# Performance work log

Hardware: AMD Instinct MI355X
Metric: run time of the kernel (lower is better)

Reference implementation:

```python
import jax, jax.numpy as jnp
import numpy as np

N_M, N_C, D, H, E, EL = 200000, 50000, 128, 64, 1000000, 100000


def gat_conv(h_src, h_dst, W_src, W_dst, a_src, a_dst, b, src, dst, n_dst):
    # PyG GATConv (heads=1): project, per-edge attention logit, segment softmax over dst, weighted scatter-sum.
    hs = h_src @ W_src                      # [Ns, H]
    hd = h_dst @ W_dst                      # [Nd, H]
    al_s = hs @ a_src                       # [Ns]
    al_d = hd @ a_dst                       # [Nd]
    alpha = jax.nn.leaky_relu(al_s[src] + al_d[dst], 0.2)   # [E]
    m = jax.ops.segment_max(alpha, dst, num_segments=n_dst)
    m = jnp.where(jnp.isfinite(m), m, 0.0)
    e = jnp.exp(alpha - m[dst])
    denom = jax.ops.segment_sum(e, dst, num_segments=n_dst)
    w = e / jnp.maximum(denom[dst], 1e-16)
    out = jax.ops.segment_sum(w[:, None] * hs[src], dst, num_segments=n_dst)
    return out + b


def setup_inputs() -> dict:
    key = jax.random.key(0)
    ks = jax.random.split(key, 32)
    p = lambda k, s: (jax.random.normal(k, s, jnp.float32) * 0.1)
    inp = {
        'x_m': jax.random.normal(ks[0], (N_M, D), jnp.float32),
        'x_c': jax.random.normal(ks[1], (N_C, D), jnp.float32),
        'src_mc': jax.random.randint(ks[2], (E,), 0, N_M, jnp.int32),
        'dst_mc': jax.random.randint(ks[3], (E,), 0, N_C, jnp.int32),
        'src_cm': jax.random.randint(ks[4], (E,), 0, N_C, jnp.int32),
        'dst_cm': jax.random.randint(ks[5], (E,), 0, N_M, jnp.int32),
        'row': jax.random.randint(ks[6], (EL,), 0, N_M, jnp.int32),
        'col': jax.random.randint(ks[7], (EL,), 0, N_C, jnp.int32),
        'W1s_mc': p(ks[8], (D, H)), 'W1d_mc': p(ks[9], (D, H)),
        'a1s_mc': p(ks[10], (H,)), 'a1d_mc': p(ks[11], (H,)), 'b1_mc': p(ks[12], (H,)),
        'W1s_cm': p(ks[13], (D, H)), 'W1d_cm': p(ks[14], (D, H)),
        'a1s_cm': p(ks[15], (H,)), 'a1d_cm': p(ks[16], (H,)), 'b1_cm': p(ks[17], (H,)),
        'W2s_mc': p(ks[18], (H, H)), 'W2d_mc': p(ks[19], (H, H)),
        'a2s_mc': p(ks[20], (H,)), 'a2d_mc': p(ks[21], (H,)), 'b2_mc': p(ks[22], (H,)),
        'W2s_cm': p(ks[23], (H, H)), 'W2d_cm': p(ks[24], (H, H)),
        'a2s_cm': p(ks[25], (H,)), 'a2d_cm': p(ks[26], (H,)), 'b2_cm': p(ks[27], (H,)),
        'Wd1': p(ks[28], (2 * H, H)), 'bd1': p(ks[29], (H,)),
        'Wd2': p(ks[30], (H, 2)), 'bd2': p(ks[31], (2,)),
    }
    return inp


def reference(x_m, x_c, src_mc, dst_mc, src_cm, dst_cm, row, col,
              W1s_mc, W1d_mc, a1s_mc, a1d_mc, b1_mc,
              W1s_cm, W1d_cm, a1s_cm, a1d_cm, b1_cm,
              W2s_mc, W2d_mc, a2s_mc, a2d_mc, b2_mc,
              W2s_cm, W2d_cm, a2s_cm, a2d_cm, b2_cm,
              Wd1, bd1, Wd2, bd2):
    # Layer 1: materials receive only via concepts->materials edges; concepts via materials->concepts.
    z_c = jax.nn.relu(gat_conv(x_m, x_c, W1s_mc, W1d_mc, a1s_mc, a1d_mc, b1_mc, src_mc, dst_mc, N_C))
    z_m = jax.nn.relu(gat_conv(x_c, x_m, W1s_cm, W1d_cm, a1s_cm, a1d_cm, b1_cm, src_cm, dst_cm, N_M))
    # Layer 2 (no activation)
    z_c2 = gat_conv(z_m, z_c, W2s_mc, W2d_mc, a2s_mc, a2d_mc, b2_mc, src_mc, dst_mc, N_C)
    z_m2 = gat_conv(z_c, z_m, W2s_cm, W2d_cm, a2s_cm, a2d_cm, b2_cm, src_cm, dst_cm, N_M)
    # Edge decoder: gather-concat + 2-layer MLP (no activation between, per source)
    z = jnp.concatenate([z_m2[row], z_c2[col]], axis=-1)   # [EL, 2H]
    z = z @ Wd1 + bd1
    z = z @ Wd2 + bd2
    return z.reshape(-1)
```

## Files before the change

### kernel.cpp

```cpp
#include <hip/hip_runtime.h>
#include <hip/hip_fp16.h>
#include <cstdint>
#include <cstddef>

typedef _Float16 f16x8 __attribute__((ext_vector_type(8)));
typedef float f32x4 __attribute__((ext_vector_type(4)));

__device__ __forceinline__ float exp_am8(float a) {
    return __builtin_amdgcn_exp2f(fmaf(a, 1.442695040888963f, -11.541560327111707f));
}

__global__ void prep_all(
    const float* __restrict__ Wa0, const float* __restrict__ Wb0, _Float16* __restrict__ P0,
    const float* __restrict__ Wa1, const float* __restrict__ Wb1, _Float16* __restrict__ P1,
    const float* __restrict__ Wd1, const float* __restrict__ bd1,
    const float* __restrict__ Wd2, const float* __restrict__ bd2,
    const float* __restrict__ b2_cm, const float* __restrict__ b2_mc,
    const float* __restrict__ W2s_mc, const float* __restrict__ a2s_mc,
    const float* __restrict__ W2d_cm, const float* __restrict__ a2d_cm,
    const float* __restrict__ W2s_cm, const float* __restrict__ a2s_cm,
    const float* __restrict__ W2d_mc, const float* __restrict__ a2d_mc,
    float* __restrict__ Wc, float* __restrict__ bc, float* __restrict__ bq,
    float4* __restrict__ foldA, float4* __restrict__ foldB,
    int* __restrict__ bcnt_base) {
    __shared__ float WcS[256];
    int b = blockIdx.x;
    int t = threadIdx.x;
    if (b < 128) {
        const float* Wa; const float* Wb; _Float16* Wp; int lb;
        if (b < 64) { Wa = Wa0; Wb = Wb0; Wp = P0; lb = b; }
        else        { Wa = Wa1; Wb = Wb1; Wp = P1; lb = b - 64; }
        constexpr int K = 128;
        constexpr int NKB = K / 32;
        int i = lb * 256 + t;
        if (i >= 128 * K) return;
        int k = i >> 7, c = i & 127;
        float v = (c < 64) ? Wa[k * 64 + c] : Wb[k * 64 + (c - 64)];
        int ct = c >> 4, lr = c & 15, kb = k >> 5, lk = (k & 31) >> 3, e = k & 7;
        Wp[((ct * NKB + kb) * 64 + (lr + 16 * lk)) * 8 + e] = (_Float16)v;
    } else if (b == 128) {
        int k = t >> 1, c = t & 1;
        float s = 0.f;
        for (int j = 0; j < 64; ++j) s += Wd1[k * 64 + j] * Wd2[j * 2 + c];
        Wc[k * 2 + c] = s;
        WcS[k * 2 + c] = s;
        if (k == 0) {
            float bv = bd2[c];
            for (int j = 0; j < 64; ++j) bv += bd1[j] * Wd2[j * 2 + c];
            bc[c] = bv;
        }
        __syncthreads();
        if (t < 2) {
            float v = 0.f;
            for (int j = 0; j < 64; ++j) v += b2_cm[j] * WcS[j * 2 + t];
            bq[t] = v;
        } else if (t < 4) {
            int cc = t - 2;
            float v = 0.f;
            for (int j = 0; j < 64; ++j) v += b2_mc[j] * WcS[(64 + j) * 2 + cc];
            bq[t] = v;
        }
        if (t < 64) {
            int j = t;
            float fa = 0.f, fd = 0.f, qx = 0.f, qy = 0.f;
            for (int cc = 0; cc < 64; ++cc) {
                float ws = W2s_mc[j * 64 + cc];
                fa += ws * a2s_mc[cc];
                qx += ws * WcS[(64 + cc) * 2 + 0];
                qy += ws * WcS[(64 + cc) * 2 + 1];
                fd += W2d_cm[j * 64 + cc] * a2d_cm[cc];
            }
            foldA[j] = make_float4(fa, fd, qx, qy);
        } else if (t < 128) {
            int j = t - 64;
            float fa = 0.f, fd = 0.f, qx = 0.f, qy = 0.f;
            for (int cc = 0; cc < 64; ++cc) {
                float ws = W2s_cm[j * 64 + cc];
                fa += ws * a2s_cm[cc];
                qx += ws * WcS[cc * 2 + 0];
                qy += ws * WcS[cc * 2 + 1];
                fd += W2d_mc[j * 64 + cc] * a2d_mc[cc];
            }
            foldB[j] = make_float4(fa, fd, qx, qy);
        }
    } else {
        bcnt_base[t] = 0;
        bcnt_base[t + 256] = 0;
    }
}

#define XPAD 72

__device__ __forceinline__ void proj_body(const float* __restrict__ X, int N,
                                          const _Float16* __restrict__ Wp,
                                          const float* __restrict__ a0v,
                                          const float* __restrict__ a1v,
                                          __half* __restrict__ out0,
                                          float* __restrict__ al0,
                                          float* __restrict__ al1,
                                          char* smem, int blk) {
    constexpr int K = 128;
    _Float16* Wlds = (_Float16*)smem;
    _Float16* Xs = (_Float16*)(smem + 32768);
    int t = threadIdx.x;
    constexpr int NV = (128 * K) / 8;
#pragma unroll
    for (int i = t; i < NV; i += 512)
        ((uint4*)Wlds)[i] = ((const uint4*)Wp)[i];

    int rt = blk * 128;
    int wv = t >> 6, lane = t & 63, lr = lane & 15, lk = lane >> 4;
    int row = rt + wv * 16 + lr;
    int xrow = t >> 4;
    int xcp = t & 15;

    f32x4 acc[8];
#pragma unroll
    for (int i = 0; i < 8; ++i) acc[i] = f32x4{0.f, 0.f, 0.f, 0.f};

    const f16x8* Wf = (const f16x8*)Wlds;
#pragma unroll
    for (int half = 0; half < 2; ++half) {
        __syncthreads();
#pragma unroll
        for (int pass = 0; pass < 4; ++pass) {
            int r = pass * 32 + xrow;
            int grow = rt + r;
            if (grow >= N) grow = N - 1;
            float4 v = *(const float4*)(X + (size_t)grow * K + half * 64 + xcp * 4);
            __half2 h01 = __floats2half2_rn(v.x, v.y);
            __half2 h23 = __floats2half2_rn(v.z, v.w);
            uint2 pk;
            pk.x = *(const unsigned int*)&h01;
            pk.y = *(const unsigned int*)&h23;
            *(uint2*)&Xs[r * XPAD + xcp * 4] = pk;
        }
        __syncthreads();
#pragma unroll
        for (int kb = 0; kb < 2; ++kb) {
            f16x8 bf = *(const f16x8*)&Xs[(wv * 16 + lr) * XPAD + kb * 32 + lk * 8];
            int kbb = half * 2 + kb;
#pragma unroll
            for (int ct = 0; ct < 8; ++ct) {
                acc[ct] = __builtin_amdgcn_mfma_f32_16x16x32_f16(
                    Wf[(ct * 4 + kbb) * 64 + lane], bf, acc[ct], 0, 0, 0);
            }
        }
    }

    float p0 = 0.f, p1 = 0.f;
#pragma unroll
    for (int ct = 0; ct < 4; ++ct) {
        float4 aq = ((const float4*)a0v)[ct * 4 + lk];
        f32x4 v = acc[ct];
        p0 += v[0] * aq.x + v[1] * aq.y + v[2] * aq.z + v[3] * aq.w;
    }
#pragma unroll
    for (int ct = 0; ct < 4; ++ct) {
        float4 aq = ((const float4*)a1v)[ct * 4 + lk];
        f32x4 v = acc[4 + ct];
        p1 += v[0] * aq.x + v[1] * aq.y + v[2] * aq.z + v[3] * aq.w;
    }
    p0 += __shfl_xor(p0, 16); p0 += __shfl_xor(p0, 32);
    p1 += __shfl_xor(p1, 16); p1 += __shfl_xor(p1, 32);
    if (row < N) {
#pragma unroll
        for (int ct = 0; ct < 4; ++ct) {
            f32x4 v = acc[ct];
            __half2 h01 = __floats2half2_rn(v[0], v[1]);
            __half2 h23 = __floats2half2_rn(v[2], v[3]);
            uint2 pk;
            pk.x = *(const unsigned int*)&h01;
            pk.y = *(const unsigned int*)&h23;
            *(uint2*)(out0 + ((size_t)row << 6) + ct * 16 + lk * 4) = pk;
        }
        if (lane < 16) { al0[row] = p0; al1[row] = p1; }
    }
}

__global__ __launch_bounds__(512) void fused_proj_hist(
    const float* __restrict__ Xm, int Nm, const _Float16* __restrict__ WpA,
    const float* __restrict__ a0A, const float* __restrict__ a1A,
    __half* __restrict__ outA, float* __restrict__ al0A, float* __restrict__ al1A, int nbm,
    const float* __restrict__ Xc, int Nc, const _Float16* __restrict__ WpB,
    const float* __restrict__ a0B, const float* __restrict__ a1B,
    __half* __restrict__ outB, float* __restrict__ al0B, float* __restrict__ al1B, int nbc,
    const int* __restrict__ dmc, int* __restrict__ bcnt_mc, int shA,
    const int* __restrict__ dcm, int* __restrict__ bcnt_cm, int shB, int E, int nblk) {
    extern __shared__ __align__(16) char smem[];
    int b = blockIdx.x;
    if (b < nbm) {
        proj_body(Xm, Nm, WpA, a0A, a1A, outA, al0A, al1A, smem, b);
        return;
    }
    b -= nbm;
    if (b < nbc) {
        proj_body(Xc, Nc, WpB, a0B, a1B, outB, al0B, al1B, smem, b);
        return;
    }
    b -= nbc;
    int* h = (int*)smem;
    const int* dst; int* bcnt; int sh; int base;
    if (b < nblk) { dst = dmc; bcnt = bcnt_mc; sh = shA; base = b * 4096; }
    else { dst = dcm; bcnt = bcnt_cm; sh = shB; base = (b - nblk) * 4096; }
    int t = threadIdx.x;
    if (t < 256) h[t] = 0;
    __syncthreads();
#pragma unroll
    for (int j = 0; j < 8; ++j) {
        int i = base + j * 512 + t;
        if (i < E) atomicAdd(&h[dst[i] >> sh], 1);
    }
    __syncthreads();
    if (t < 256) {
        int c = h[t];
        if (c > 0) atomicAdd(&bcnt[t], c);
    }
}

__global__ void bucket_scan(const int* __restrict__ bcntA, int nbkA,
                            int* __restrict__ bbaseA, int* __restrict__ bcurA,
                            int* __restrict__ offA, int nA,
                            const int* __restrict__ bcntB, int nbkB,
                            int* __restrict__ bbaseB, int* __restrict__ bcurB,
                            int* __restrict__ offB, int nB, int E) {
    int t = threadIdx.x;
    if (t == 0) {
        int run = 0;
        for (int i = 0; i < nbkA; ++i) { bbaseA[i] = run; bcurA[i] = run; run += bcntA[i]; }
        bbaseA[nbkA] = run;
        offA[nA] = E;
    }
    if (t == 64) {
        int run = 0;
        for (int i = 0; i < nbkB; ++i) { bbaseB[i] = run; bcurB[i] = run; run += bcntB[i]; }
        bbaseB[nbkB] = run;
        offB[nB] = E;
    }
}

__global__ __launch_bounds__(256) void bucket_scatter(
    const int* __restrict__ srcA, const int* __restrict__ dstA,
    int* __restrict__ bcurA, unsigned* __restrict__ pairsA,
    const int* __restrict__ srcB, const int* __restrict__ dstB,
    int* __restrict__ bcurB, unsigned* __restrict__ pairsB,
    int E, int nblkA, int shA, int shB, int srcbits) {
    __shared__ int bcnt[256];
    __shared__ int bbase[256];
    const int* src; const int* dst; int* bcur; unsigned* pairs; int sh; int base;
    if ((int)blockIdx.x < nblkA) {
        src = srcA; dst = dstA; bcur = bcurA; pairs = pairsA; sh = shA;
        base = blockIdx.x * 4096;
    } else {
        src = srcB; dst = dstB; bcur = bcurB; pairs = pairsB; sh = shB;
        base = (blockIdx.x - nblkA) * 4096;
    }
    int t = threadIdx.x;
    int msk = (1 << sh) - 1;
    bcnt[t] = 0;
    __syncthreads();
    int sreg[16], dreg[16];
#pragma unroll
    for (int j = 0; j < 16; ++j) {
        int i = base + j * 256 + t;
        if (i < E) {
            sreg[j] = src[i];
            dreg[j] = dst[i];
            atomicAdd(&bcnt[dreg[j] >> sh], 1);
        } else {
            dreg[j] = -1;
        }
    }
    __syncthreads();
    {
        int c = bcnt[t];
        int g = (c > 0) ? atomicAdd(&bcur[t], c) : 0;
        bbase[t] = g;
        bcnt[t] = 0;
    }
    __syncthreads();
#pragma unroll
    for (int j = 0; j < 16; ++j) {
        if (dreg[j] >= 0) {
            int b = dreg[j] >> sh;
            int r = atomicAdd(&bcnt[b], 1);
            pairs[bbase[b] + r] = ((unsigned)(dreg[j] & msk) << srcbits) | (unsigned)sreg[j];
        }
    }
}

__global__ __launch_bounds__(256) void bucket_expand2(
    const unsigned* __restrict__ pairsA, const int* __restrict__ bbaseA, int nA,
    int* __restrict__ offA, int* __restrict__ csrA, int shA, int nbA,
    const unsigned* __restrict__ pairsB, const int* __restrict__ bbaseB, int nB,
    int* __restrict__ offB, int* __restrict__ csrB, int shB, int srcbits) {
    __shared__ int lcnt[1024];
    __shared__ int red[256];
    const unsigned* pairs; const int* bbase; int n; int* off; int* csr; int sh; int b;
    if ((int)blockIdx.x < nbA) {
        pairs = pairsA; bbase = bbaseA; n = nA; off = offA; csr = csrA; sh = shA;
        b = blockIdx.x;
    } else {
        pairs = pairsB; bbase = bbaseB; n = nB; off = offB; csr = csrB; sh = shB;
        b = blockIdx.x - nbA;
    }
    int dpb = 1 << sh;
    int d0 = b << sh;
    int t = threadIdx.x;
    unsigned smask = (1u << srcbits) - 1u;
    for (int dl = t; dl < dpb; dl += 256) lcnt[dl] = 0;
    __syncthreads();
    int pbeg = bbase[b], pend = bbase[b + 1];
    for (int i = pbeg + t; i < pend; i += 256)
        atomicAdd(&lcnt[pairs[i] >> srcbits], 1);
    __syncthreads();
    int per = (dpb + 255) >> 8;
    int i0 = t * per;
    int s = 0;
    for (int j = 0; j < per; ++j) {
        int dl = i0 + j;
        if (dl < dpb) s += lcnt[dl];
    }
    red[t] = s;
    __syncthreads();
    for (int st = 1; st < 256; st <<= 1) {
        int tmp = (t >= st) ? red[t - st] : 0;
        __syncthreads();
        red[t] += tmp;
        __syncthreads();
    }
    int run = pbeg + red[t] - s;
    for (int j = 0; j < per; ++j) {
        int dl = i0 + j;
        if (dl < dpb) {
            int c = lcnt[dl];
            if (d0 + dl < n) off[d0 + dl] = run;
            lcnt[dl] = run;
            run += c;
        }
    }
    __syncthreads();
    for (int i = pbeg + t; i < pend; i += 256) {
        unsigned p = pairs[i];
        int dl = (int)(p >> srcbits);
        int pos = atomicAdd(&lcnt[dl], 1);
        csr[pos] = (int)(p & smask);
    }
}

#define AGG_CAP 64
#define AGG_PAD 66

__global__ __launch_bounds__(256) void gat_aggregate9f(
    const int* __restrict__ off0, const int* __restrict__ csr0,
    const __half* __restrict__ hs0, const float* __restrict__ als0,
    const float* __restrict__ ald0, const float* __restrict__ bias0,
    const float4* __restrict__ fold0, float* __restrict__ als2_0,
    float* __restrict__ ald2_0, float2* __restrict__ q2_0, int n0,
    const int* __restrict__ off1, const int* __restrict__ csr1,
    const __half* __restrict__ hs1, const float* __restrict__ als1,
    const float* __restrict__ ald1, const float* __restrict__ bias1,
    const float4* __restrict__ fold1, float* __restrict__ als2_1,
    float* __restrict__ ald2_1, float2* __restrict__ q2_1, int n1,
    int nb0) {
    __shared__ uint2 wP[16][AGG_PAD];
    int t = threadIdx.x;
    int slot = t >> 4;
    int sub = t & 15;

    const int* off; const int* csr; const __half* hs; const float* als;
    const float* ald; const float* bias; const float4* fold;
    float* als2; float* ald2; float2* q2; int nd; int b;
    if (blockIdx.x < (unsigned)nb0) {
        b = blockIdx.x;
        off = off0; csr = csr0; hs = hs0; als = als0; ald = ald0; bias = bias0;
        fold = fold0; als2 = als2_0; ald2 = ald2_0; q2 = q2_0; nd = n0;
    } else {
        b = blockIdx.x - nb0;
        off = off1; csr = csr1; hs = hs1; als = als1; ald = ald1; bias = bias1;
        fold = fold1; als2 = als2_1; ald2 = ald2_1; q2 = q2_1; nd = n1;
    }
    int d = b * 16 + slot;
    bool active = d < nd;
    int beg = 0, deg = 0;
    float aldv = 0.f;
    if (active) {
        beg = off[d];
        deg = off[d + 1] - beg;
        aldv = ald[d];
    }
    float4 bl4 = ((const float4*)bias)[sub];
    uint2* WP = wP[slot];

    float sum = 0.f;
    for (int i = sub; i < deg; i += 16) {
        int s = csr[beg + i];
        float a = als[s] + aldv;
        a = (a >= 0.f) ? a : 0.2f * a;
        float w = exp_am8(a);
        sum += w;
        if (i < AGG_CAP) {
            __half hw = __float2half_rn(w);
            __half2 h2 = __half2half2(hw);
            WP[i] = make_uint2(*(const unsigned int*)&h2, (unsigned int)s);
        }
    }
    sum += __shfl_xor(sum, 1);
    sum += __shfl_xor(sum, 2);
    sum += __shfl_xor(sum, 4);
    sum += __shfl_xor(sum, 8);
    float inv = 1.f / fmaxf(sum, 1e-16f);

    int dc = deg < AGG_CAP ? deg : AGG_CAP;
    const uint2* hs4 = (const uint2*)hs;
    __half2 z = __floats2half2_rn(0.f, 0.f);
    __half2 aA = z, aB = z, aC = z, aD = z;
    int i = 0;
    for (; i + 8 <= dc; i += 8) {
        uint4 q0 = *(const uint4*)&WP[i];
        uint4 q1 = *(const uint4*)&WP[i + 2];
        uint4 q2r = *(const uint4*)&WP[i + 4];
        uint4 q3 = *(const uint4*)&WP[i + 6];
        uint2 v0 = hs4[(size_t)q0.y * 16 + sub];
        uint2 v1 = hs4[(size_t)q0.w * 16 + sub];
        uint2 v2 = hs4[(size_t)q1.y * 16 + sub];
        uint2 v3 = hs4[(size_t)q1.w * 16 + sub];
        uint2 v4 = hs4[(size_t)q2r.y * 16 + sub];
        uint2 v5 = hs4[(size_t)q2r.w * 16 + sub];
        uint2 v6 = hs4[(size_t)q3.y * 16 + sub];
        uint2 v7 = hs4[(size_t)q3.w * 16 + sub];
        aA = __hfma2(*(const __half2*)&q0.x, *(const __half2*)&v0.x, aA);
        aB = __hfma2(*(const __half2*)&q0.x, *(const __half2*)&v0.y, aB);
        aC = __hfma2(*(const __half2*)&q0.z, *(const __half2*)&v1.x, aC);
        aD = __hfma2(*(const __half2*)&q0.z, *(const __half2*)&v1.y, aD);
        aA = __hfma2(*(const __half2*)&q1.x, *(const __half2*)&v2.x, aA);
        aB = __hfma2(*(const __half2*)&q1.x, *(const __half2*)&v2.y, aB);
        aC = __hfma2(*(const __half2*)&q1.z, *(const __half2*)&v3.x, aC);
        aD = __hfma2(*(const __half2*)&q1.z, *(const __half2*)&v3.y, aD);
        aA = __hfma2(*(const __half2*)&q2r.x, *(const __half2*)&v4.x, aA);
        aB = __hfma2(*(const __half2*)&q2r.x, *(const __half2*)&v4.y, aB);
        aC = __hfma2(*(const __half2*)&q2r.z, *(const __half2*)&v5.x, aC);
        aD = __hfma2(*(const __half2*)&q2r.z, *(const __half2*)&v5.y, aD);
        aA = __hfma2(*(const __half2*)&q3.x, *(const __half2*)&v6.x, aA);
        aB = __hfma2(*(const __half2*)&q3.x, *(const __half2*)&v6.y, aB);
        aC = __hfma2(*(const __half2*)&q3.z, *(const __half2*)&v7.x, aC);
        aD = __hfma2(*(const __half2*)&q3.z, *(const __half2*)&v7.y, aD);
    }
    for (; i + 2 <= dc; i += 2) {
        uint4 q = *(const uint4*)&WP[i];
        uint2 v0 = hs4[(size_t)q.y * 16 + sub];
        uint2 v1 = hs4[(size_t)q.w * 16 + sub];
        aA = __hfma2(*(const __half2*)&q.x, *(const __half2*)&v0.x, aA);
        aB = __hfma2(*(const __half2*)&q.x, *(const __half2*)&v0.y, aB);
        aC = __hfma2(*(const __half2*)&q.z, *(const __half2*)&v1.x, aC);
        aD = __hfma2(*(const __half2*)&q.z, *(const __half2*)&v1.y, aD);
    }
    if (i < dc) {
        uint2 u = WP[i];
        uint2 v = hs4[(size_t)u.y * 16 + sub];
        aA = __hfma2(*(const __half2*)&u.x, *(const __half2*)&v.x, aA);
        aB = __hfma2(*(const __half2*)&u.x, *(const __half2*)&v.y, aB);
    }
    for (int j = AGG_CAP; j < deg; ++j) {
        int s = csr[beg + j];
        float a = als[s] + aldv;
        a = (a >= 0.f) ? a : 0.2f * a;
        __half hw = __float2half_rn(exp_am8(a));
        __half2 w2 = __half2half2(hw);
        uint2 v = hs4[(size_t)s * 16 + sub];
        aA = __hfma2(w2, *(const __half2*)&v.x, aA);
        aB = __hfma2(w2, *(const __half2*)&v.y, aB);
    }
    float2 fA = __half22float2(aA);
    float2 fB = __half22float2(aB);
    float2 fC = __half22float2(aC);
    float2 fD = __half22float2(aD);
    float o0 = (fA.x + fC.x) * inv + bl4.x;
    float o1 = (fA.y + fC.y) * inv + bl4.y;
    float o2 = (fB.x + fD.x) * inv + bl4.z;
    float o3 = (fB.y + fD.y) * inv + bl4.w;
    if (deg == 0) { o0 = bl4.x; o1 = bl4.y; o2 = bl4.z; o3 = bl4.w; }
    o0 = fmaxf(o0, 0.f); o1 = fmaxf(o1, 0.f);
    o2 = fmaxf(o2, 0.f); o3 = fmaxf(o3, 0.f);

    float4 f0 = fold[4 * sub + 0];
    float4 f1 = fold[4 * sub + 1];
    float4 f2 = fold[4 * sub + 2];
    float4 f3 = fold[4 * sub + 3];
    float a0 = o0 * f0.x + o1 * f1.x + o2 * f2.x + o3 * f3.x;
    float a1 = o0 * f0.y + o1 * f1.y + o2 * f2.y + o3 * f3.y;
    float a2 = o0 * f0.z + o1 * f1.z + o2 * f2.z + o3 * f3.z;
    float a3 = o0 * f0.w + o1 * f1.w + o2 * f2.w + o3 * f3.w;
#pragma unroll
    for (int o = 1; o < 16; o <<= 1) {
        a0 += __shfl_xor(a0, o);
        a1 += __shfl_xor(a1, o);
        a2 += __shfl_xor(a2, o);
        a3 += __shfl_xor(a3, o);
    }
    if (active && sub == 0) {
        als2[d] = a0;
        ald2[d] = a1;
        q2[d] = make_float2(a2, a3);
    }
}

__global__ __launch_bounds__(256) void gat_aggregate10p(
    const int* __restrict__ off0, const int* __restrict__ csr0,
    const float2* __restrict__ q0, const float* __restrict__ als0,
    const float* __restrict__ ald0, const float2* __restrict__ bqp,
    float2* __restrict__ out0, int n0,
    const int* __restrict__ off1, const int* __restrict__ csr1,
    const float2* __restrict__ q1, const float* __restrict__ als1,
    const float* __restrict__ ald1,
    float2* __restrict__ out1, int n1,
    int nb0) {
    const int* off; const int* csr; const float2* qt; const float* als;
    const float* ald; float2 bq; float2* outp; int nd; int b;
    if (blockIdx.x < (unsigned)nb0) {
        b = blockIdx.x;
        off = off0; csr = csr0; qt = q0; als = als0; ald = ald0; bq = bqp[1];
        outp = out0; nd = n0;
    } else {
        b = blockIdx.x - nb0;
        off = off1; csr = csr1; qt = q1; als = als1; ald = ald1; bq = bqp[0];
        outp = out1; nd = n1;
    }
    int d = b * 256 + threadIdx.x;
    if (d >= nd) return;
    int beg = off[d], end = off[d + 1];
    float aldv = ald[d];
    float sum = 0.f, ax = 0.f, ay = 0.f;
    int i = beg;
    for (; i + 2 <= end; i += 2) {
        int s0 = csr[i], s1 = csr[i + 1];
        float a0 = als[s0] + aldv;
        float a1 = als[s1] + aldv;
        float2 v0 = qt[s0];
        float2 v1 = qt[s1];
        a0 = (a0 >= 0.f) ? a0 : 0.2f * a0;
        a1 = (a1 >= 0.f) ? a1 : 0.2f * a1;
        float w0 = exp_am8(a0);
        float w1 = exp_am8(a1);
        sum += w0 + w1;
        ax = fmaf(w0, v0.x, ax); ay = fmaf(w0, v0.y, ay);
        ax = fmaf(w1, v1.x, ax); ay = fmaf(w1, v1.y, ay);
    }
    if (i < end) {
        int s = csr[i];
        float a = als[s] + aldv;
        a = (a >= 0.f) ? a : 0.2f * a;
        float w = exp_am8(a);
        float2 v = qt[s];
        sum += w;
        ax = fmaf(w, v.x, ax); ay = fmaf(w, v.y, ay);
    }
    float inv = 1.f / fmaxf(sum, 1e-16f);
    outp[d] = make_float2(ax * inv + bq.x, ay * inv + bq.y);
}

__global__ __launch_bounds__(256) void decoder4_kernel(const int* __restrict__ row,
                                                       const int* __restrict__ col,
                                                       const float2* __restrict__ pm,
                                                       const float2* __restrict__ pc,
                                                       const float* __restrict__ bc,
                                                       float* __restrict__ out, int EL) {
    int e = blockIdx.x * 256 + threadIdx.x;
    if (e >= EL) return;
    float2 a = pm[row[e]];
    float2 b = pc[col[e]];
    *(float2*)(out + 2 * (size_t)e) = make_float2(a.x + b.x + bc[0], a.y + b.y + bc[1]);
}

extern "C" void kernel_launch(void* const* d_in, const int* in_sizes, int n_in,
                              void* d_out, int out_size, void* d_ws, size_t ws_size,
                              hipStream_t stream) {
    const int D = 128;
    const float* x_m    = (const float*)d_in[0];
    const float* x_c    = (const float*)d_in[1];
    const int*   src_mc = (const int*)d_in[2];
    const int*   dst_mc = (const int*)d_in[3];
    const int*   src_cm = (const int*)d_in[4];
    const int*   dst_cm = (const int*)d_in[5];
    const int*   rowi   = (const int*)d_in[6];
    const int*   coli   = (const int*)d_in[7];
    const float* W1s_mc = (const float*)d_in[8];
    const float* W1d_mc = (const float*)d_in[9];
    const float* a1s_mc = (const float*)d_in[10];
    const float* a1d_mc = (const float*)d_in[11];
    const float* b1_mc  = (const float*)d_in[12];
    const float* W1s_cm = (const float*)d_in[13];
    const float* W1d_cm = (const float*)d_in[14];
    const float* a1s_cm = (const float*)d_in[15];
    const float* a1d_cm = (const float*)d_in[16];
    const float* b1_cm  = (const float*)d_in[17];
    const float* W2s_mc = (const float*)d_in[18];
    const float* W2d_mc = (const float*)d_in[19];
    const float* a2s_mc = (const float*)d_in[20];
    const float* a2d_mc = (const float*)d_in[21];
    const float* b2_mc  = (const float*)d_in[22];
    const float* W2s_cm = (const float*)d_in[23];
    const float* W2d_cm = (const float*)d_in[24];
    const float* a2s_cm = (const float*)d_in[25];
    const float* a2d_cm = (const float*)d_in[26];
    const float* b2_cm  = (const float*)d_in[27];
    const float* Wd1    = (const float*)d_in[28];
    const float* bd1    = (const float*)d_in[29];
    const float* Wd2    = (const float*)d_in[30];
    const float* bd2    = (const float*)d_in[31];

    const int N_M = in_sizes[0] / D;
    const int N_C = in_sizes[1] / D;
    const int E   = in_sizes[2];
    const int EL  = in_sizes[6];
    float* out = (float*)d_out;

    uint8_t* base = (uint8_t*)d_ws;
    size_t off = 0;
    auto carve = [&](size_t bytes) -> void* {
        void* p = base + off;
        off += (bytes + 255) & ~(size_t)255;
        return p;
    };
    __half* hsA_h = (__half*)carve((size_t)N_M * 64 * 2);
    __half* hsB_h = (__half*)carve((size_t)N_C * 64 * 2);
    float2* qA    = (float2*)carve((size_t)N_M * 8);
    float2* qB    = (float2*)carve((size_t)N_C * 8);
    float2* pm_m  = (float2*)carve((size_t)N_M * 8);
    float2* pm_c  = (float2*)carve((size_t)N_C * 8);
    float* als_mc = (float*)carve((size_t)N_M * 4);
    float* ald_cm = (float*)carve((size_t)N_M * 4);
    float* als_cm = (float*)carve((size_t)N_C * 4);
    float* ald_mc = (float*)carve((size_t)N_C * 4);
    float* als2_mc = (float*)carve((size_t)N_M * 4);
    float* ald2_cm = (float*)carve((size_t)N_M * 4);
    float* als2_cm = (float*)carve((size_t)N_C * 4);
    float* ald2_mc = (float*)carve((size_t)N_C * 4);
    int* off_mc = (int*)carve((size_t)(N_C + 1) * 4);
    int* off_cm = (int*)carve((size_t)(N_M + 1) * 4);
    int* csr_mc = (int*)carve((size_t)E * 4);
    int* csr_cm = (int*)carve((size_t)E * 4);
    unsigned* pairs_mc = (unsigned*)carve((size_t)E * 4);
    unsigned* pairs_cm = (unsigned*)carve((size_t)E * 4);
    int* bcnt_base = (int*)carve(512 * 4);
    int* bcnt_mc = bcnt_base;
    int* bcnt_cm = bcnt_base + 256;
    int* bbase_mc = (int*)carve(257 * 4);
    int* bbase_cm = (int*)carve(257 * 4);
    int* bcur_mc = (int*)carve(256 * 4);
    int* bcur_cm = (int*)carve(256 * 4);
    _Float16* wp1A = (_Float16*)carve(128 * 128 * 2);
    _Float16* wp1B = (_Float16*)carve(128 * 128 * 2);
    float* Wc = (float*)carve(256 * 4);
    float* bc = (float*)carve(256);
    float* bq = (float*)carve(256);
    float2* bq2 = (float2*)bq;
    float4* foldA = (float4*)carve(64 * 16);
    float4* foldB = (float4*)carve(64 * 16);

    int shA = 0; while (((N_C + (1 << shA) - 1) >> shA) > 256) shA++;
    int shB = 0; while (((N_M + (1 << shB) - 1) >> shB) > 256) shB++;
    int nbkA = (N_C + (1 << shA) - 1) >> shA;
    int nbkB = (N_M + (1 << shB) - 1) >> shB;
    int maxN = N_M > N_C ? N_M : N_C;
    int srcbits = 1; while ((1 << srcbits) < maxN) srcbits++;

    prep_all<<<130, 256, 0, stream>>>(W1s_mc, W1d_cm, wp1A, W1s_cm, W1d_mc, wp1B,
                                      Wd1, bd1, Wd2, bd2, b2_cm, b2_mc,
                                      W2s_mc, a2s_mc, W2d_cm, a2d_cm,
                                      W2s_cm, a2s_cm, W2d_mc, a2d_mc,
                                      Wc, bc, bq, foldA, foldB, bcnt_base);

    int nbm = (N_M + 127) / 128;
    int nbc = (N_C + 127) / 128;
    int nblk = (E + 4095) / 4096;
    size_t smem_bytes = 32768 + (size_t)128 * XPAD * 2;
    fused_proj_hist<<<nbm + nbc + 2 * nblk, 512, smem_bytes, stream>>>(
        x_m, N_M, wp1A, a1s_mc, a1d_cm, hsA_h, als_mc, ald_cm, nbm,
        x_c, N_C, wp1B, a1s_cm, a1d_mc, hsB_h, als_cm, ald_mc, nbc,
        dst_mc, bcnt_mc, shA, dst_cm, bcnt_cm, shB, E, nblk);

    bucket_scan<<<1, 128, 0, stream>>>(bcnt_mc, nbkA, bbase_mc, bcur_mc, off_mc, N_C,
                                       bcnt_cm, nbkB, bbase_cm, bcur_cm, off_cm, N_M, E);
    bucket_scatter<<<2 * nblk, 256, 0, stream>>>(
        src_mc, dst_mc, bcur_mc, pairs_mc,
        src_cm, dst_cm, bcur_cm, pairs_cm, E, nblk, shA, shB, srcbits);
    bucket_expand2<<<nbkA + nbkB, 256, 0, stream>>>(
        pairs_mc, bbase_mc, N_C, off_mc, csr_mc, shA, nbkA,
        pairs_cm, bbase_cm, N_M, off_cm, csr_cm, shB, srcbits);

    int nb_c16 = (N_C + 15) / 16;
    int nb_m16 = (N_M + 15) / 16;

    gat_aggregate9f<<<nb_c16 + nb_m16, 256, 0, stream>>>(
        off_mc, csr_mc, hsA_h, als_mc, ald_mc, b1_mc, foldB, als2_cm, ald2_mc, qB, N_C,
        off_cm, csr_cm, hsB_h, als_cm, ald_cm, b1_cm, foldA, als2_mc, ald2_cm, qA, N_M,
        nb_c16);

    int nb_c256 = (N_C + 255) / 256;
    int nb_m256 = (N_M + 255) / 256;
    gat_aggregate10p<<<nb_c256 + nb_m256, 256, 0, stream>>>(
        off_mc, csr_mc, qA, als2_mc, ald2_mc, bq2, pm_c, N_C,
        off_cm, csr_cm, qB, als2_cm, ald2_cm, pm_m, N_M, nb_c256);

    decoder4_kernel<<<(EL + 255) / 256, 256, 0, stream>>>(rowi, coli, pm_m, pm_c, bc, out, EL);
}
```

Before: 198.8 us.

## Keep projection weights in registers and split output columns across waves

Measured after the change: 197.4 us. Within noise of the previous version (-0.7%).

```diff
diff --git a/kernel.cpp b/kernel.cpp
--- a/kernel.cpp
+++ b/kernel.cpp
@@ -100,25 +100,26 @@
                                           float* __restrict__ al1,
                                           char* smem, int blk) {
     constexpr int K = 128;
-    _Float16* Wlds = (_Float16*)smem;
-    _Float16* Xs = (_Float16*)(smem + 32768);
+    _Float16* Xs = (_Float16*)smem;
+    float* red0 = (float*)(smem + 128 * XPAD * 2);
+    float* red1 = red0 + 128;
     int t = threadIdx.x;
-    constexpr int NV = (128 * K) / 8;
-#pragma unroll
-    for (int i = t; i < NV; i += 512)
-        ((uint4*)Wlds)[i] = ((const uint4*)Wp)[i];
-
+    int wv = t >> 6, lane = t & 63, lr = lane & 15, lk = lane >> 4;
     int rt = blk * 128;
-    int wv = t >> 6, lane = t & 63, lr = lane & 15, lk = lane >> 4;
-    int row = rt + wv * 16 + lr;
     int xrow = t >> 4;
     int xcp = t & 15;
 
+    f16x8 wfr[4];
+#pragma unroll
+    for (int kbb = 0; kbb < 4; ++kbb)
+        wfr[kbb] = ((const f16x8*)Wp)[(wv * 4 + kbb) * 64 + lane];
+
+    if (t < 128) { red0[t] = 0.f; red1[t] = 0.f; }
+
     f32x4 acc[8];
 #pragma unroll
     for (int i = 0; i < 8; ++i) acc[i] = f32x4{0.f, 0.f, 0.f, 0.f};
 
-    const f16x8* Wf = (const f16x8*)Wlds;
 #pragma unroll
     for (int half = 0; half < 2; ++half) {
         __syncthreads();
@@ -137,44 +138,40 @@
         }
         __syncthreads();
 #pragma unroll
-        for (int kb = 0; kb < 2; ++kb) {
-            f16x8 bf = *(const f16x8*)&Xs[(wv * 16 + lr) * XPAD + kb * 32 + lk * 8];
-            int kbb = half * 2 + kb;
-#pragma unroll
-            for (int ct = 0; ct < 8; ++ct) {
-                acc[ct] = __builtin_amdgcn_mfma_f32_16x16x32_f16(
-                    Wf[(ct * 4 + kbb) * 64 + lane], bf, acc[ct], 0, 0, 0);
+        for (int rt8 = 0; rt8 < 8; ++rt8) {
+#pragma unroll
+            for (int kb = 0; kb < 2; ++kb) {
+                f16x8 bf = *(const f16x8*)&Xs[(rt8 * 16 + lr) * XPAD + kb * 32 + lk * 8];
+                acc[rt8] = __builtin_amdgcn_mfma_f32_16x16x32_f16(
+                    wfr[half * 2 + kb], bf, acc[rt8], 0, 0, 0);
             }
         }
     }
 
-    float p0 = 0.f, p1 = 0.f;
-#pragma unroll
-    for (int ct = 0; ct < 4; ++ct) {
-        float4 aq = ((const float4*)a0v)[ct * 4 + lk];
-        f32x4 v = acc[ct];
-        p0 += v[0] * aq.x + v[1] * aq.y + v[2] * aq.z + v[3] * aq.w;
-    }
-#pragma unroll
-    for (int ct = 0; ct < 4; ++ct) {
-        float4 aq = ((const float4*)a1v)[ct * 4 + lk];
-        f32x4 v = acc[4 + ct];
-        p1 += v[0] * aq.x + v[1] * aq.y + v[2] * aq.z + v[3] * aq.w;
-    }
-    p0 += __shfl_xor(p0, 16); p0 += __shfl_xor(p0, 32);
-    p1 += __shfl_xor(p1, 16); p1 += __shfl_xor(p1, 32);
-    if (row < N) {
-#pragma unroll
-        for (int ct = 0; ct < 4; ++ct) {
-            f32x4 v = acc[ct];
+    bool is_s = wv < 4;
+    float4 aq = is_s ? ((const float4*)a0v)[wv * 4 + lk]
+                     : ((const float4*)a1v)[(wv - 4) * 4 + lk];
+    float* red = is_s ? red0 : red1;
+#pragma unroll
+    for (int rt8 = 0; rt8 < 8; ++rt8) {
+        f32x4 v = acc[rt8];
+        float p = v[0] * aq.x + v[1] * aq.y + v[2] * aq.z + v[3] * aq.w;
+        p += __shfl_xor(p, 16); p += __shfl_xor(p, 32);
+        if (lane < 16) atomicAdd(&red[rt8 * 16 + lr], p);
+        int row = rt + rt8 * 16 + lr;
+        if (is_s && row < N) {
             __half2 h01 = __floats2half2_rn(v[0], v[1]);
             __half2 h23 = __floats2half2_rn(v[2], v[3]);
             uint2 pk;
             pk.x = *(const unsigned int*)&h01;
             pk.y = *(const unsigned int*)&h23;
-            *(uint2*)(out0 + ((size_t)row << 6) + ct * 16 + lk * 4) = pk;
-        }
-        if (lane < 16) { al0[row] = p0; al1[row] = p1; }
+            *(uint2*)(out0 + ((size_t)row << 6) + wv * 16 + lk * 4) = pk;
+        }
+    }
+    __syncthreads();
+    if (t < 128) {
+        int row = rt + t;
+        if (row < N) { al0[row] = red0[t]; al1[row] = red1[t]; }
     }
 }
 
@@ -674,7 +671,7 @@
     int nbm = (N_M + 127) / 128;
     int nbc = (N_C + 127) / 128;
     int nblk = (E + 4095) / 4096;
-    size_t smem_bytes = 32768 + (size_t)128 * XPAD * 2;
+    size_t smem_bytes = (size_t)128 * XPAD * 2 + 256 * 4;
     fused_proj_hist<<<nbm + nbc + 2 * nblk, 512, smem_bytes, stream>>>(
         x_m, N_M, wp1A, a1s_mc, a1d_cm, hsA_h, als_mc, ald_cm, nbm,
         x_c, N_C, wp1B, a1s_cm, a1d_mc, hsB_h, als_cm, ald_mc, nbc,
```
